# Performance work log

Measured on AMD Instinct MI355X. Metric: run time of the kernel, lower is better.

The kernel has to match this reference:

```python
import jax, jax.numpy as jnp
import numpy as np

NEG_SLOPE = 0.2  # PyG GATConv default LeakyReLU slope


def _prelu(x, a):
    return jnp.where(x >= 0, x, a * x)


def _gat_conv(h, src, dst, W, a_s, a_d, b, n):
    """Single-head PyG GATConv (self-loops already in src/dst).
    h: [N,D] node feats; src/dst: [E'] edge endpoints (edge j->i as src=j, dst=i).
    """
    g = h @ W                                    # [N, D]
    es = g @ a_s                                 # [N] alpha contribution of source nodes
    ed = g @ a_d                                 # [N] alpha contribution of dest nodes
    e = jax.nn.leaky_relu(es[src] + ed[dst], negative_slope=NEG_SLOPE)  # [E']
    # segment softmax over incoming edges of each destination node
    m = jax.ops.segment_max(e, dst, num_segments=n)      # [N]
    w = jnp.exp(e - m[dst])                              # [E']
    z = jax.ops.segment_sum(w, dst, num_segments=n)      # [N] (>0: self-loops present)
    alpha = w / z[dst]                                   # [E']
    out = jax.ops.segment_sum(alpha[:, None] * g[src], dst, num_segments=n)  # [N, D]
    return out + b


def setup_inputs() -> dict:
    key = jax.random.key(0)
    ks = jax.random.split(key, 16)
    N, E, D = 50000, 800000, 128
    s = 1.0 / np.sqrt(D)
    inp = {
        "x": jnp.arange(N, dtype=jnp.int32),
        "edge_index": jax.random.randint(ks[0], (2, E), 0, N, dtype=jnp.int32),
        "edge_weight": jax.random.uniform(ks[1], (E,), dtype=jnp.float32),
        "emb": jax.random.normal(ks[2], (N, D), dtype=jnp.float32) * 0.1,
    }
    for i, k0 in zip((1, 2, 3), (3, 6, 9)):
        inp[f"W{i}"] = jax.random.normal(ks[k0], (D, D), dtype=jnp.float32) * s
        inp[f"as{i}"] = jax.random.normal(ks[k0 + 1], (D,), dtype=jnp.float32) * s
        inp[f"ad{i}"] = jax.random.normal(ks[k0 + 2], (D,), dtype=jnp.float32) * s
        inp[f"b{i}"] = jnp.zeros((D,), dtype=jnp.float32)
        inp[f"p{i}"] = jnp.full((1,), 0.25, dtype=jnp.float32)  # PReLU init
    inp["Wo"] = jax.random.normal(ks[12], (D, D), dtype=jnp.float32) * s
    inp["bo"] = jnp.zeros((D,), dtype=jnp.float32)
    return inp


def reference(x, edge_index, edge_weight, emb,
              W1, as1, ad1, b1, p1,
              W2, as2, ad2, b2, p2,
              W3, as3, ad3, b3, p3,
              Wo, bo):
    # edge_weight is accepted but unused (never passed to GATConv in the source).
    n = x.shape[0]
    loop = jnp.arange(n, dtype=edge_index.dtype)
    src = jnp.concatenate([edge_index[0], loop])  # add_self_loops=True
    dst = jnp.concatenate([edge_index[1], loop])
    h = emb[x]                                    # pre_embs lookup
    # Dropout(0.3) is eval-mode identity.
    h = _prelu(_gat_conv(h, src, dst, W1, as1, ad1, b1, n), p1)
    h = _prelu(_gat_conv(h, src, dst, W2, as2, ad2, b2, n), p2)
    h = _prelu(_gat_conv(h, src, dst, W3, as3, ad3, b3, n), p3)
    return h @ Wo + bo
```

## Files before the change

### kernel.cpp

```cpp
#include <hip/hip_runtime.h>
#include <cstdint>
#include <cstddef>


#define NEG_SLOPE 0.2f

__global__ void deg_init_kernel(int* __restrict__ deg, int N) {
    int i = blockIdx.x * blockDim.x + threadIdx.x;
    if (i < N) deg[i] = 1;
}

__global__ void hist_kernel(const int* __restrict__ ei, int* __restrict__ deg, int E) {
    int e = blockIdx.x * blockDim.x + threadIdx.x;
    if (e < E) atomicAdd(&deg[ei[E + e]], 1);
}

__global__ void scan1_kernel(const int* __restrict__ deg, int* __restrict__ off,
                             int* __restrict__ bsum, int N) {
    __shared__ int lds[256];
    int base = blockIdx.x * 1024;
    int t = threadIdx.x;
    int v[4]; int s = 0;
#pragma unroll
    for (int j = 0; j < 4; j++) {
        int idx = base + t * 4 + j;
        v[j] = (idx < N) ? deg[idx] : 0;
        s += v[j];
    }
    lds[t] = s;
    __syncthreads();
    for (int o = 1; o < 256; o <<= 1) {
        int add = (t >= o) ? lds[t - o] : 0;
        __syncthreads();
        lds[t] += add;
        __syncthreads();
    }
    int run = lds[t] - s;
    if (t == 255) bsum[blockIdx.x] = lds[255];
#pragma unroll
    for (int j = 0; j < 4; j++) {
        int idx = base + t * 4 + j;
        if (idx < N) off[idx] = run;
        run += v[j];
    }
}

__global__ void scan2_kernel(int* __restrict__ bsum, int nblk) {
    __shared__ int lds[256];
    int t = threadIdx.x;
    int v = (t < nblk) ? bsum[t] : 0;
    lds[t] = v;
    __syncthreads();
    for (int o = 1; o < 256; o <<= 1) {
        int add = (t >= o) ? lds[t - o] : 0;
        __syncthreads();
        lds[t] += add;
        __syncthreads();
    }
    if (t < nblk) bsum[t] = lds[t] - v;
}

__global__ void scan3_kernel(int* __restrict__ off, int* __restrict__ cursor,
                             const int* __restrict__ bsum, int N, int E) {
    int base = blockIdx.x * 1024;
    int t = threadIdx.x;
    int add = bsum[blockIdx.x];
#pragma unroll
    for (int j = 0; j < 4; j++) {
        int idx = base + t * 4 + j;
        if (idx < N) {
            int v = off[idx] + add;
            off[idx] = v;
            cursor[idx] = v;
        }
    }
    if (blockIdx.x == 0 && t == 0) off[N] = E + N;
}

__global__ void fill_kernel(const int* __restrict__ ei, int* __restrict__ cursor,
                            int* __restrict__ srcs, int E, int N) {
    int t = blockIdx.x * blockDim.x + threadIdx.x;
    if (t < E) {
        int s = ei[t];
        int d = ei[E + t];
        int pos = atomicAdd(&cursor[d], 1);
        srcs[pos] = s;
    } else if (t < E + N) {
        int i = t - E;
        int pos = atomicAdd(&cursor[i], 1);
        srcs[pos] = i;
    }
}

__global__ __launch_bounds__(256) void gemm128_kernel(
        const float* __restrict__ A, const int* __restrict__ rowidx,
        const float* __restrict__ W, const float* __restrict__ bias,
        const float* __restrict__ avs, const float* __restrict__ avd,
        float* __restrict__ C, float* __restrict__ es, float* __restrict__ ed,
        int M) {
    __shared__ float As[64][36];
    __shared__ float Bs[32][128];
    int tid = threadIdx.x;
    int row0 = blockIdx.x * 64;
    int ry = tid >> 4;
    int cx = tid & 15;
    float acc[4][8];
#pragma unroll
    for (int i = 0; i < 4; i++)
#pragma unroll
        for (int j = 0; j < 8; j++) acc[i][j] = 0.f;

    for (int k0 = 0; k0 < 128; k0 += 32) {
        if (k0) __syncthreads();
#pragma unroll
        for (int i = 0; i < 2; i++) {
            int f = tid + i * 256;
            int r = f >> 3, c4 = f & 7;
            int gr = row0 + r;
            float4 v = make_float4(0.f, 0.f, 0.f, 0.f);
            if (gr < M) {
                int ar = rowidx ? rowidx[gr] : gr;
                v = ((const float4*)(A + (size_t)ar * 128 + k0))[c4];
            }
            *(float4*)&As[r][c4 * 4] = v;
        }
#pragma unroll
        for (int i = 0; i < 4; i++) {
            int f = tid + i * 256;
            int kk = f >> 5, c4 = f & 31;
            ((float4*)&Bs[kk][0])[c4] = ((const float4*)(W + (size_t)(k0 + kk) * 128))[c4];
        }
        __syncthreads();
#pragma unroll
        for (int k = 0; k < 32; k++) {
            float a0 = As[ry * 4 + 0][k];
            float a1 = As[ry * 4 + 1][k];
            float a2 = As[ry * 4 + 2][k];
            float a3 = As[ry * 4 + 3][k];
            float4 b0 = ((float4*)&Bs[k][0])[cx * 2];
            float4 b1 = ((float4*)&Bs[k][0])[cx * 2 + 1];
            float bv[8] = {b0.x, b0.y, b0.z, b0.w, b1.x, b1.y, b1.z, b1.w};
#pragma unroll
            for (int j = 0; j < 8; j++) {
                acc[0][j] += a0 * bv[j];
                acc[1][j] += a1 * bv[j];
                acc[2][j] += a2 * bv[j];
                acc[3][j] += a3 * bv[j];
            }
        }
    }
    float bv[8];
#pragma unroll
    for (int j = 0; j < 8; j++) bv[j] = bias ? bias[cx * 8 + j] : 0.f;
#pragma unroll
    for (int rr = 0; rr < 4; rr++) {
        int r = row0 + ry * 4 + rr;
        if (r >= M) continue;
        float* crow = C + (size_t)r * 128 + cx * 8;
        ((float4*)crow)[0] = make_float4(acc[rr][0] + bv[0], acc[rr][1] + bv[1],
                                         acc[rr][2] + bv[2], acc[rr][3] + bv[3]);
        ((float4*)crow)[1] = make_float4(acc[rr][4] + bv[4], acc[rr][5] + bv[5],
                                         acc[rr][6] + bv[6], acc[rr][7] + bv[7]);
    }
    if (es) {
        float vs[8], vd[8];
#pragma unroll
        for (int j = 0; j < 8; j++) { vs[j] = avs[cx * 8 + j]; vd[j] = avd[cx * 8 + j]; }
#pragma unroll
        for (int rr = 0; rr < 4; rr++) {
            float ps = 0.f, pd = 0.f;
#pragma unroll
            for (int j = 0; j < 8; j++) {
                ps += acc[rr][j] * vs[j];
                pd += acc[rr][j] * vd[j];
            }
#pragma unroll
            for (int o = 8; o; o >>= 1) {
                ps += __shfl_xor(ps, o);
                pd += __shfl_xor(pd, o);
            }
            int r = row0 + ry * 4 + rr;
            if (cx == 0 && r < M) { es[r] = ps; ed[r] = pd; }
        }
    }
}

__global__ void aggregate_kernel(const float* __restrict__ g, const float* __restrict__ es,
                                 const float* __restrict__ ed, const int* __restrict__ off,
                                 const int* __restrict__ srcs, const float* __restrict__ b,
                                 const float* __restrict__ p, float* __restrict__ hout, int N) {
    int gt = blockIdx.x * blockDim.x + threadIdx.x;
    int i = gt >> 6, lane = gt & 63;
    if (i >= N) return;
    int s0 = off[i], s1 = off[i + 1];
    int cnt = s1 - s0;
    float edi = ed[i];
    float acc0 = 0.f, acc1 = 0.f, z = 0.f;
    if (cnt <= 64) {
        int sj = 0;
        float e = -3.0e38f;
        if (lane < cnt) {
            sj = srcs[s0 + lane];
            float t = es[sj] + edi;
            e = (t >= 0.f) ? t : NEG_SLOPE * t;
        }
        float m = e;
#pragma unroll
        for (int o = 32; o; o >>= 1) m = fmaxf(m, __shfl_xor(m, o));
        float w = (lane < cnt) ? __expf(e - m) : 0.f;
        z = w;
#pragma unroll
        for (int o = 32; o; o >>= 1) z += __shfl_xor(z, o);
        for (int j = 0; j < cnt; ++j) {
            int s = __shfl(sj, j);
            float wj = __shfl(w, j);
            float2 gv = *(const float2*)(g + (size_t)s * 128 + lane * 2);
            acc0 += wj * gv.x;
            acc1 += wj * gv.y;
        }
    } else {
        float m = -3.0e38f;
        for (int j = s0 + lane; j < s1; j += 64) {
            float t = es[srcs[j]] + edi;
            t = (t >= 0.f) ? t : NEG_SLOPE * t;
            m = fmaxf(m, t);
        }
#pragma unroll
        for (int o = 32; o; o >>= 1) m = fmaxf(m, __shfl_xor(m, o));
        for (int j = s0; j < s1; ++j) {
            int s = srcs[j];
            float t = es[s] + edi;
            t = (t >= 0.f) ? t : NEG_SLOPE * t;
            float w = __expf(t - m);
            z += w;
            float2 gv = *(const float2*)(g + (size_t)s * 128 + lane * 2);
            acc0 += w * gv.x;
            acc1 += w * gv.y;
        }
    }
    float pv = p[0];
    float inv = 1.f / z;
    float2 bb = *(const float2*)(b + lane * 2);
    float o0 = acc0 * inv + bb.x;
    float o1 = acc1 * inv + bb.y;
    o0 = (o0 >= 0.f) ? o0 : pv * o0;
    o1 = (o1 >= 0.f) ? o1 : pv * o1;
    *(float2*)(hout + (size_t)i * 128 + lane * 2) = make_float2(o0, o1);
}

extern "C" void kernel_launch(void* const* d_in, const int* in_sizes, int n_in,
                              void* d_out, int out_size, void* d_ws, size_t ws_size,
                              hipStream_t stream) {
    const int*   x   = (const int*)d_in[0];
    const int*   ei  = (const int*)d_in[1];
    const float* emb = (const float*)d_in[3];
    const float* W1  = (const float*)d_in[4];
    const float* as1 = (const float*)d_in[5];
    const float* ad1 = (const float*)d_in[6];
    const float* b1  = (const float*)d_in[7];
    const float* p1  = (const float*)d_in[8];
    const float* W2  = (const float*)d_in[9];
    const float* as2 = (const float*)d_in[10];
    const float* ad2 = (const float*)d_in[11];
    const float* b2  = (const float*)d_in[12];
    const float* p2  = (const float*)d_in[13];
    const float* W3  = (const float*)d_in[14];
    const float* as3 = (const float*)d_in[15];
    const float* ad3 = (const float*)d_in[16];
    const float* b3  = (const float*)d_in[17];
    const float* p3  = (const float*)d_in[18];
    const float* Wo  = (const float*)d_in[19];
    const float* bo  = (const float*)d_in[20];

    const int N = in_sizes[0];
    const int E = in_sizes[2];

    char* wp = (char*)d_ws;
    auto carve = [&](size_t bytes) {
        char* r = wp;
        wp += (bytes + 255) & ~(size_t)255;
        return r;
    };
    float* h0     = (float*)carve((size_t)N * 128 * 4);
    float* h1     = (float*)carve((size_t)N * 128 * 4);
    float* g      = (float*)carve((size_t)N * 128 * 4);
    float* es     = (float*)carve((size_t)N * 4);
    float* ed     = (float*)carve((size_t)N * 4);
    int*   deg    = (int*)carve((size_t)N * 4);
    int*   off    = (int*)carve((size_t)(N + 1) * 4);
    int*   cursor = (int*)carve((size_t)N * 4);
    int*   srcs   = (int*)carve((size_t)(E + N) * 4);
    int*   bsum   = (int*)carve(1024 * 4);
    (void)ws_size; (void)n_in;

    deg_init_kernel<<<(N + 255) / 256, 256, 0, stream>>>(deg, N);
    hist_kernel<<<(E + 255) / 256, 256, 0, stream>>>(ei, deg, E);
    int nblk = (N + 1023) / 1024;
    scan1_kernel<<<nblk, 256, 0, stream>>>(deg, off, bsum, N);
    scan2_kernel<<<1, 256, 0, stream>>>(bsum, nblk);
    scan3_kernel<<<nblk, 256, 0, stream>>>(off, cursor, bsum, N, E);
    fill_kernel<<<(E + N + 255) / 256, 256, 0, stream>>>(ei, cursor, srcs, E, N);

    int gemm_grid = (N + 63) / 64;
    int wave_grid = (N * 64 + 255) / 256;

    gemm128_kernel<<<gemm_grid, 256, 0, stream>>>(emb, x, W1, nullptr, as1, ad1, g, es, ed, N);
    aggregate_kernel<<<wave_grid, 256, 0, stream>>>(g, es, ed, off, srcs, b1, p1, h1, N);
    gemm128_kernel<<<gemm_grid, 256, 0, stream>>>(h1, nullptr, W2, nullptr, as2, ad2, g, es, ed, N);
    aggregate_kernel<<<wave_grid, 256, 0, stream>>>(g, es, ed, off, srcs, b2, p2, h0, N);
    gemm128_kernel<<<gemm_grid, 256, 0, stream>>>(h0, nullptr, W3, nullptr, as3, ad3, g, es, ed, N);
    aggregate_kernel<<<wave_grid, 256, 0, stream>>>(g, es, ed, off, srcs, b3, p3, h1, N);
    gemm128_kernel<<<gemm_grid, 256, 0, stream>>>(h1, nullptr, Wo, bo, nullptr, nullptr,
                                                  (float*)d_out, nullptr, nullptr, N);
}
```

Before: 548.9 us.

## Split wavefront into half-waves for float4 edge gathers and restructure GEMM A loads

The aggregation kernel now splits each 64-lane wavefront into two halves. Each half processes alternate edges with float4 loads of the 128-wide feature row, and the loop is unrolled to issue four independent gathers per half per iteration. The halves are combined with a cross-half shuffle at the end. This aims to raise memory-level parallelism in the gather-dominated aggregation. The GEMM drops the A tile from shared memory and reads A rows straight from global memory as float4, doubles the W k-tile to 64, and changes the column mapping so shared-memory reads use float4. The trade-off is uncoalesced, repeated A reads across the 16 column threads of each row, which rely on cache hits.

```diff
diff --git a/kernel.cpp b/kernel.cpp
--- a/kernel.cpp
+++ b/kernel.cpp
@@ -4,6 +4,8 @@
 
 
 #define NEG_SLOPE 0.2f
+
+__device__ __forceinline__ float leaky(float t) { return t >= 0.f ? t : NEG_SLOPE * t; }
 
 __global__ void deg_init_kernel(int* __restrict__ deg, int N) {
     int i = blockIdx.x * blockDim.x + threadIdx.x;
@@ -98,74 +100,81 @@
         const float* __restrict__ avs, const float* __restrict__ avd,
         float* __restrict__ C, float* __restrict__ es, float* __restrict__ ed,
         int M) {
-    __shared__ float As[64][36];
-    __shared__ float Bs[32][128];
+    __shared__ float Bs[64][128];
     int tid = threadIdx.x;
     int row0 = blockIdx.x * 64;
     int ry = tid >> 4;
     int cx = tid & 15;
+
+    const float* arow[4];
+#pragma unroll
+    for (int rr = 0; rr < 4; rr++) {
+        int gr = row0 + ry * 4 + rr;
+        int ar = 0;
+        if (gr < M) ar = rowidx ? rowidx[gr] : gr;
+        arow[rr] = A + (size_t)ar * 128;
+    }
+
     float acc[4][8];
 #pragma unroll
     for (int i = 0; i < 4; i++)
 #pragma unroll
         for (int j = 0; j < 8; j++) acc[i][j] = 0.f;
 
-    for (int k0 = 0; k0 < 128; k0 += 32) {
+    for (int k0 = 0; k0 < 128; k0 += 64) {
         if (k0) __syncthreads();
 #pragma unroll
-        for (int i = 0; i < 2; i++) {
-            int f = tid + i * 256;
-            int r = f >> 3, c4 = f & 7;
-            int gr = row0 + r;
-            float4 v = make_float4(0.f, 0.f, 0.f, 0.f);
-            if (gr < M) {
-                int ar = rowidx ? rowidx[gr] : gr;
-                v = ((const float4*)(A + (size_t)ar * 128 + k0))[c4];
-            }
-            *(float4*)&As[r][c4 * 4] = v;
-        }
-#pragma unroll
-        for (int i = 0; i < 4; i++) {
+        for (int i = 0; i < 8; i++) {
             int f = tid + i * 256;
             int kk = f >> 5, c4 = f & 31;
-            ((float4*)&Bs[kk][0])[c4] = ((const float4*)(W + (size_t)(k0 + kk) * 128))[c4];
-        }
-        __syncthreads();
-#pragma unroll
-        for (int k = 0; k < 32; k++) {
-            float a0 = As[ry * 4 + 0][k];
-            float a1 = As[ry * 4 + 1][k];
-            float a2 = As[ry * 4 + 2][k];
-            float a3 = As[ry * 4 + 3][k];
-            float4 b0 = ((float4*)&Bs[k][0])[cx * 2];
-            float4 b1 = ((float4*)&Bs[k][0])[cx * 2 + 1];
-            float bv[8] = {b0.x, b0.y, b0.z, b0.w, b1.x, b1.y, b1.z, b1.w};
-#pragma unroll
-            for (int j = 0; j < 8; j++) {
-                acc[0][j] += a0 * bv[j];
-                acc[1][j] += a1 * bv[j];
-                acc[2][j] += a2 * bv[j];
-                acc[3][j] += a3 * bv[j];
+            *(float4*)&Bs[kk][c4 * 4] = ((const float4*)(W + (size_t)(k0 + kk) * 128))[c4];
+        }
+        __syncthreads();
+#pragma unroll 2
+        for (int k4 = 0; k4 < 16; k4++) {
+            float4 a4[4];
+#pragma unroll
+            for (int rr = 0; rr < 4; rr++)
+                a4[rr] = *(const float4*)(arow[rr] + k0 + k4 * 4);
+#pragma unroll
+            for (int kk = 0; kk < 4; kk++) {
+                float4 b0 = *(const float4*)&Bs[k4 * 4 + kk][cx * 4];
+                float4 b1 = *(const float4*)&Bs[k4 * 4 + kk][64 + cx * 4];
+#pragma unroll
+                for (int rr = 0; rr < 4; rr++) {
+                    float a = (kk == 0) ? a4[rr].x : (kk == 1) ? a4[rr].y
+                              : (kk == 2) ? a4[rr].z : a4[rr].w;
+                    acc[rr][0] += a * b0.x; acc[rr][1] += a * b0.y;
+                    acc[rr][2] += a * b0.z; acc[rr][3] += a * b0.w;
+                    acc[rr][4] += a * b1.x; acc[rr][5] += a * b1.y;
+                    acc[rr][6] += a * b1.z; acc[rr][7] += a * b1.w;
+                }
             }
         }
     }
     float bv[8];
 #pragma unroll
-    for (int j = 0; j < 8; j++) bv[j] = bias ? bias[cx * 8 + j] : 0.f;
+    for (int j = 0; j < 4; j++) {
+        bv[j]     = bias ? bias[cx * 4 + j] : 0.f;
+        bv[4 + j] = bias ? bias[64 + cx * 4 + j] : 0.f;
+    }
 #pragma unroll
     for (int rr = 0; rr < 4; rr++) {
         int r = row0 + ry * 4 + rr;
         if (r >= M) continue;
-        float* crow = C + (size_t)r * 128 + cx * 8;
-        ((float4*)crow)[0] = make_float4(acc[rr][0] + bv[0], acc[rr][1] + bv[1],
-                                         acc[rr][2] + bv[2], acc[rr][3] + bv[3]);
-        ((float4*)crow)[1] = make_float4(acc[rr][4] + bv[4], acc[rr][5] + bv[5],
-                                         acc[rr][6] + bv[6], acc[rr][7] + bv[7]);
+        float* crow = C + (size_t)r * 128;
+        *(float4*)(crow + cx * 4) = make_float4(acc[rr][0] + bv[0], acc[rr][1] + bv[1],
+                                                acc[rr][2] + bv[2], acc[rr][3] + bv[3]);
+        *(float4*)(crow + 64 + cx * 4) = make_float4(acc[rr][4] + bv[4], acc[rr][5] + bv[5],
+                                                     acc[rr][6] + bv[6], acc[rr][7] + bv[7]);
     }
     if (es) {
         float vs[8], vd[8];
 #pragma unroll
-        for (int j = 0; j < 8; j++) { vs[j] = avs[cx * 8 + j]; vd[j] = avd[cx * 8 + j]; }
+        for (int j = 0; j < 4; j++) {
+            vs[j] = avs[cx * 4 + j];          vd[j] = avd[cx * 4 + j];
+            vs[4 + j] = avs[64 + cx * 4 + j]; vd[4 + j] = avd[64 + cx * 4 + j];
+        }
 #pragma unroll
         for (int rr = 0; rr < 4; rr++) {
             float ps = 0.f, pd = 0.f;
@@ -195,14 +204,15 @@
     int s0 = off[i], s1 = off[i + 1];
     int cnt = s1 - s0;
     float edi = ed[i];
-    float acc0 = 0.f, acc1 = 0.f, z = 0.f;
+    int half = lane >> 5, l32 = lane & 31;
+    float4 acc = make_float4(0.f, 0.f, 0.f, 0.f);
+    float z = 0.f;
     if (cnt <= 64) {
         int sj = 0;
         float e = -3.0e38f;
         if (lane < cnt) {
             sj = srcs[s0 + lane];
-            float t = es[sj] + edi;
-            e = (t >= 0.f) ? t : NEG_SLOPE * t;
+            e = leaky(es[sj] + edi);
         }
         float m = e;
 #pragma unroll
@@ -211,41 +221,64 @@
         z = w;
 #pragma unroll
         for (int o = 32; o; o >>= 1) z += __shfl_xor(z, o);
-        for (int j = 0; j < cnt; ++j) {
-            int s = __shfl(sj, j);
-            float wj = __shfl(w, j);
-            float2 gv = *(const float2*)(g + (size_t)s * 128 + lane * 2);
-            acc0 += wj * gv.x;
-            acc1 += wj * gv.y;
+        int jb = 0;
+        for (; jb + 8 <= cnt; jb += 8) {
+            int j0 = jb + half, j1 = jb + 2 + half, j2 = jb + 4 + half, j3 = jb + 6 + half;
+            int   sa = __shfl(sj, j0), sb = __shfl(sj, j1);
+            int   sc = __shfl(sj, j2), sd = __shfl(sj, j3);
+            float wa = __shfl(w, j0),  wb = __shfl(w, j1);
+            float wc = __shfl(w, j2),  wd = __shfl(w, j3);
+            float4 ga = *(const float4*)(g + (size_t)sa * 128 + l32 * 4);
+            float4 gb = *(const float4*)(g + (size_t)sb * 128 + l32 * 4);
+            float4 gc = *(const float4*)(g + (size_t)sc * 128 + l32 * 4);
+            float4 gd = *(const float4*)(g + (size_t)sd * 128 + l32 * 4);
+            acc.x += wa * ga.x + wb * gb.x + wc * gc.x + wd * gd.x;
+            acc.y += wa * ga.y + wb * gb.y + wc * gc.y + wd * gd.y;
+            acc.z += wa * ga.z + wb * gb.z + wc * gc.z + wd * gd.z;
+            acc.w += wa * ga.w + wb * gb.w + wc * gc.w + wd * gd.w;
+        }
+        for (; jb < cnt; jb += 2) {
+            int j = jb + half;
+            int   sa = __shfl(sj, j);
+            float wa = __shfl(w, j);
+            float4 ga = *(const float4*)(g + (size_t)sa * 128 + l32 * 4);
+            acc.x += wa * ga.x; acc.y += wa * ga.y;
+            acc.z += wa * ga.z; acc.w += wa * ga.w;
         }
     } else {
         float m = -3.0e38f;
-        for (int j = s0 + lane; j < s1; j += 64) {
-            float t = es[srcs[j]] + edi;
-            t = (t >= 0.f) ? t : NEG_SLOPE * t;
-            m = fmaxf(m, t);
-        }
+        for (int jj = s0 + lane; jj < s1; jj += 64)
+            m = fmaxf(m, leaky(es[srcs[jj]] + edi));
 #pragma unroll
         for (int o = 32; o; o >>= 1) m = fmaxf(m, __shfl_xor(m, o));
-        for (int j = s0; j < s1; ++j) {
+        for (int j = s0 + half; j < s1; j += 2) {
             int s = srcs[j];
-            float t = es[s] + edi;
-            t = (t >= 0.f) ? t : NEG_SLOPE * t;
-            float w = __expf(t - m);
-            z += w;
-            float2 gv = *(const float2*)(g + (size_t)s * 128 + lane * 2);
-            acc0 += w * gv.x;
-            acc1 += w * gv.y;
-        }
-    }
-    float pv = p[0];
-    float inv = 1.f / z;
-    float2 bb = *(const float2*)(b + lane * 2);
-    float o0 = acc0 * inv + bb.x;
-    float o1 = acc1 * inv + bb.y;
-    o0 = (o0 >= 0.f) ? o0 : pv * o0;
-    o1 = (o1 >= 0.f) ? o1 : pv * o1;
-    *(float2*)(hout + (size_t)i * 128 + lane * 2) = make_float2(o0, o1);
+            float wj = __expf(leaky(es[s] + edi) - m);
+            z += wj;
+            float4 gv = *(const float4*)(g + (size_t)s * 128 + l32 * 4);
+            acc.x += wj * gv.x; acc.y += wj * gv.y;
+            acc.z += wj * gv.z; acc.w += wj * gv.w;
+        }
+        z += __shfl_xor(z, 32);
+    }
+    acc.x += __shfl_xor(acc.x, 32);
+    acc.y += __shfl_xor(acc.y, 32);
+    acc.z += __shfl_xor(acc.z, 32);
+    acc.w += __shfl_xor(acc.w, 32);
+    if (half == 0) {
+        float pv = p[0];
+        float inv = 1.f / z;
+        float4 bb = *(const float4*)(b + l32 * 4);
+        float o0 = acc.x * inv + bb.x;
+        float o1 = acc.y * inv + bb.y;
+        float o2 = acc.z * inv + bb.z;
+        float o3 = acc.w * inv + bb.w;
+        o0 = (o0 >= 0.f) ? o0 : pv * o0;
+        o1 = (o1 >= 0.f) ? o1 : pv * o1;
+        o2 = (o2 >= 0.f) ? o2 : pv * o2;
+        o3 = (o3 >= 0.f) ? o3 : pv * o3;
+        *(float4*)(hout + (size_t)i * 128 + l32 * 4) = make_float4(o0, o1, o2, o3);
+    }
 }
 
 extern "C" void kernel_launch(void* const* d_in, const int* in_sizes, int n_in,
```

Result: faster. 515.8 us (-6.0%).
